# Performance work log

Hardware: AMD Instinct MI355X
Metric: run time of the kernel (lower is better)

Reference implementation:

```python
import jax, jax.numpy as jnp
import numpy as np

B, L, N, H, HU = 512, 16, 10000, 128, 128

def _rn(k, shape, s=0.05):
    return jax.random.normal(k, shape, jnp.float32) * s

def setup_inputs():
    ks = jax.random.split(jax.random.key(0), 26)
    return dict(
        x=jax.random.normal(ks[0], (B, 2), jnp.float32),
        t0_res=jax.random.normal(ks[1], (B, 1), jnp.float32),
        node_inputs=jax.random.normal(ks[2], (B, 2 * L, N), jnp.float32),
        tau_inputs=jax.random.normal(ks[3], (B, L, 1), jnp.float32),
        end=jax.random.normal(ks[4], (B, 2), jnp.float32),
        coords=jax.random.normal(ks[5], (B, 2 * L, 2), jnp.float32),
        Wx1=_rn(ks[6], (1, 2)), Wx2=_rn(ks[7], (H, 1)), bx2=_rn(ks[8], (H,)),
        Wres=_rn(ks[9], (H, 1)), bres=_rn(ks[10], (H,)),
        Wnode=_rn(ks[11], (H, N)),
        Wtau=_rn(ks[12], (H, 1)), btau=_rn(ks[13], (H,)),
        Wend1=_rn(ks[14], (1, 2)), Wend2=_rn(ks[15], (H, 1)), bend2=_rn(ks[16], (H,)),
        Wcoord=_rn(ks[17], (H, 2)),
        lstm_Wih=_rn(ks[18], (7, 4 * H, H)), lstm_Whh=_rn(ks[19], (7, 4 * H, H)),
        lstm_bih=_rn(ks[20], (7, 4 * H)), lstm_bhh=_rn(ks[21], (7, 4 * H)),
        head_W1=_rn(ks[22], (7, HU, H)), head_b1=_rn(ks[23], (7, HU)),
        head_W2=_rn(ks[24], (7, 1, HU)), head_b2=_rn(ks[25], (7, 1)),
    )

def _lstm_last(s, Wih, Whh, bih, bhh):
    # s: [T, B, H] (time-first, like torch LSTM default). PyTorch gate order: i, f, g, o.
    h0 = jnp.zeros((s.shape[1], Whh.shape[1]), s.dtype)
    def step(carry, xt):
        h, c = carry
        g = xt @ Wih.T + h @ Whh.T + (bih + bhh)
        i, f, gg, o = jnp.split(g, 4, axis=-1)
        c = jax.nn.sigmoid(f) * c + jax.nn.sigmoid(i) * jnp.tanh(gg)
        h = jax.nn.sigmoid(o) * jnp.tanh(c)
        return (h, c), None
    (h, _), _ = jax.lax.scan(step, (h0, h0), s)
    return h  # last output == last hidden state

def _forward(x, t0_res, node_inputs, tau_inputs, end, coords,
             Wx1, Wx2, bx2, Wres, bres, Wnode, Wtau, btau,
             Wend1, Wend2, bend2, Wcoord,
             lstm_Wih, lstm_Whh, lstm_bih, lstm_bhh,
             head_W1, head_b1, head_W2, head_b2):
    xh = jnp.tanh((x @ Wx1.T) @ Wx2.T + bx2)        # [B,H]
    t0h = jnp.tanh(t0_res @ Wres.T + bres)          # [B,H]
    nodeh = node_inputs @ Wnode.T                   # [B,2L,H] (dominant memory-bound GEMM)
    tauh = jnp.tanh(tau_inputs @ Wtau.T + btau)     # [B,L,H]
    endh = (end @ Wend1.T) @ Wend2.T + bend2        # [B,H]
    coordh = coords @ Wcoord.T                      # [B,2L,H]
    ne, no = nodeh[:, 0::2], nodeh[:, 1::2]         # even/odd walk nodes [B,L,H]
    ce, co = coordh[:, 0::2], coordh[:, 1::2]
    def interleave(parts):  # k x [B,L,H] -> time-first [k*L, B, H], per-step order preserved
        s = jnp.stack(parts, axis=2)
        return jnp.swapaxes(s.reshape(s.shape[0], -1, s.shape[-1]), 0, 1)
    pre = jnp.stack([xh, t0h], axis=0)  # [2,B,H]
    suf = endh[None]                    # [1,B,H]
    seqs = [
        jnp.concatenate([pre, interleave([tauh, ne, ce, no, co]), suf], 0),  # all        T=5L+3
        jnp.concatenate([pre, interleave([tauh]), suf], 0),                  # time       T=L+3
        jnp.swapaxes(nodeh, 0, 1),                                           # node       T=2L
        jnp.swapaxes(coordh, 0, 1),                                          # coord      T=2L
        jnp.concatenate([pre, interleave([tauh, ne, no]), suf], 0),          # node_time  T=3L+3
        interleave([ne, ce, no, co]),                                        # node_coord T=4L
        jnp.concatenate([pre, interleave([tauh, ce, co]), suf], 0),          # time_coord T=3L+3
    ]
    outs = []
    for k, s in enumerate(seqs):
        h = _lstm_last(s, lstm_Wih[k], lstm_Whh[k], lstm_bih[k], lstm_bhh[k])
        outs.append(jnp.tanh(h @ head_W1[k].T + head_b1[k]) @ head_W2[k].T + head_b2[k])
    return tuple(outs)  # matches torch return order: all, time, node, coord, node_time, node_coord, time_coord

def reference(x, t0_res, node_inputs, tau_inputs, end, coords,
              Wx1, Wx2, bx2, Wres, bres, Wnode, Wtau, btau,
              Wend1, Wend2, bend2, Wcoord,
              lstm_Wih, lstm_Whh, lstm_bih, lstm_bhh,
              head_W1, head_b1, head_W2, head_b2):
    return _forward(x, t0_res, node_inputs, tau_inputs, end, coords,
                    Wx1, Wx2, bx2, Wres, bres, Wnode, Wtau, btau,
                    Wend1, Wend2, bend2, Wcoord,
                    lstm_Wih, lstm_Whh, lstm_bih, lstm_bhh,
                    head_W1, head_b1, head_W2, head_b2)
```

## Files before the change

kernel.cpp:

```cpp
#include <hip/hip_runtime.h>
#include <hip/hip_fp16.h>

typedef _Float16 f16;
typedef _Float16 f16x8 __attribute__((ext_vector_type(8)));
typedef float f32x4 __attribute__((ext_vector_type(4)));

#define NB 512
#define NL 16
#define NK 10000
#define NH 128
#define NSF 316
#define NT 79

__device__ __forceinline__ float fast_exp2(float x) {
#if __has_builtin(__builtin_amdgcn_exp2f)
  return __builtin_amdgcn_exp2f(x);
#else
  return exp2f(x);
#endif
}
__device__ __forceinline__ float fast_rcp(float x) {
#if __has_builtin(__builtin_amdgcn_rcpf)
  return __builtin_amdgcn_rcpf(x);
#else
  return 1.f / x;
#endif
}
__device__ __forceinline__ float sigf(float x) {
  return fast_rcp(1.f + fast_exp2(-1.44269504f * x));
}
__device__ __forceinline__ float tanh_fast(float x) {
  return 2.f * fast_rcp(1.f + fast_exp2(-2.88539008f * x)) - 1.f;
}

__global__ void prep_kernel(
    const float* __restrict__ x, const float* __restrict__ t0,
    const float* __restrict__ tau, const float* __restrict__ endi,
    const float* __restrict__ coords,
    const float* __restrict__ Wx1, const float* __restrict__ Wx2,
    const float* __restrict__ bx2, const float* __restrict__ Wres,
    const float* __restrict__ bres, const float* __restrict__ Wnode,
    const float* __restrict__ Wtau, const float* __restrict__ btau,
    const float* __restrict__ Wend1, const float* __restrict__ Wend2,
    const float* __restrict__ bend2, const float* __restrict__ Wcoord,
    const float* __restrict__ Wih, const float* __restrict__ Whh,
    const float* __restrict__ bih, const float* __restrict__ bhh,
    f16* __restrict__ xh, f16* __restrict__ t0h, f16* __restrict__ endh,
    f16* __restrict__ tauh, f16* __restrict__ coordh, f16* __restrict__ Wf,
    f16* __restrict__ Wih16, f16* __restrict__ Whh16, float* __restrict__ bsum) {
  const int tid0 = blockIdx.x * blockDim.x + threadIdx.x;
  const int stride = gridDim.x * blockDim.x;

  const int nWf = NSF * 4096;
  const int nW = 7 * 512 * NH;
  const int nb = 7 * 512;
  const int nxh = NB * NH;
  const int ntau = NB * NL * NH;
  const int nco = NB * 2 * NL * NH;

  for (int i = tid0; i < nWf; i += stride) {
    const int s = i >> 12, r = i & 4095;
    const int nt = r >> 9, l2 = r & 511;
    const int lane = l2 >> 3, e = l2 & 7;
    const int kg = lane >> 4, lr = lane & 15;
    const int col = nt * 16 + lr;
    const int k = s * 32 + kg * 8 + e;
    Wf[i] = (k < NK) ? (f16)Wnode[(size_t)col * NK + k] : (f16)0.f;
  }
  for (int i = tid0; i < nW; i += stride) {
    Wih16[i] = (f16)Wih[i];
    Whh16[i] = (f16)Whh[i];
  }
  for (int i = tid0; i < nb; i += stride) bsum[i] = bih[i] + bhh[i];
  for (int i = tid0; i < nxh; i += stride) {
    const int b = i >> 7, h = i & 127;
    const float s = x[2 * b] * Wx1[0] + x[2 * b + 1] * Wx1[1];
    xh[i] = (f16)tanhf(s * Wx2[h] + bx2[h]);
    t0h[i] = (f16)tanhf(t0[b] * Wres[h] + bres[h]);
    const float e = endi[2 * b] * Wend1[0] + endi[2 * b + 1] * Wend1[1];
    endh[i] = (f16)(e * Wend2[h] + bend2[h]);
  }
  for (int i = tid0; i < ntau; i += stride) {
    const int h = i & 127, bl = i >> 7;
    tauh[i] = (f16)tanhf(tau[bl] * Wtau[h] + btau[h]);
  }
  for (int i = tid0; i < nco; i += stride) {
    const int h = i & 127, br = i >> 7;
    coordh[i] = (f16)(coords[2 * br] * Wcoord[2 * h] +
                      coords[2 * br + 1] * Wcoord[2 * h + 1]);
  }
}

__global__ __launch_bounds__(512, 2) void node_gemm(const float* __restrict__ A,
                                                    const f16* __restrict__ Wf,
                                                    f16* __restrict__ Cn) {
  __shared__ char lds[4][32768];
  const int tid = threadIdx.x;
  const int w = tid >> 6, l = tid & 63;
  const int lr = l & 15, kg = l >> 4;
  const int r0 = blockIdx.x * 64;
  char* lds0 = &lds[0][0];

  const char* ap[4];
  int bnd[4], wdo[4];
#pragma unroll
  for (int i = 0; i < 4; i++) {
    const int row = w * 8 + i * 2 + (l >> 5);
    const int off = (l & 31) * 16;
    ap[i] = (const char*)A + (size_t)(r0 + row) * 40000 + off;
    bnd[i] = 39984 - off;
    wdo[i] = row * 512 + (off ^ ((row & 7) << 4));
  }

  const int kw = w & 1, cp = w >> 1;
  int rdoA[4][2][2];
#pragma unroll
  for (int rg = 0; rg < 4; rg++) {
    const int row = rg * 16 + lr;
    const int sw = (row & 7) << 4;
#pragma unroll
    for (int ks = 0; ks < 2; ks++)
#pragma unroll
      for (int h = 0; h < 2; h++)
        rdoA[rg][ks][h] =
            row * 512 + ((kw * 256 + ks * 128 + kg * 32 + h * 16) ^ sw);
  }

  f32x4 acc[4][2];
#pragma unroll
  for (int rg = 0; rg < 4; rg++)
#pragma unroll
    for (int j = 0; j < 2; j++) {
      f32x4 z = {0.f, 0.f, 0.f, 0.f};
      acc[rg][j] = z;
    }

  auto loadA = [&](int t, f32x4 (&r)[4]) {
    const int tb = t * 512;
#pragma unroll
    for (int i = 0; i < 4; i++) {
      const int off = tb < bnd[i] ? tb : bnd[i];
      r[i] = *(const f32x4*)(ap[i] + off);
    }
  };

  auto dswrite = [&](int t, const f32x4 (&r)[4]) {
    char* db = lds0 + (t & 3) * 32768;
#pragma unroll
    for (int i = 0; i < 4; i++) *(f32x4*)(db + wdo[i]) = r[i];
  };

  auto loadB = [&](int t, f16x8 (&B)[2][2]) {
    const f16* bp = Wf + (size_t)(4 * t + 2 * kw) * 4096 + cp * 1024 + l * 8;
#pragma unroll
    for (int j = 0; j < 2; j++)
#pragma unroll
      for (int ks = 0; ks < 2; ks++)
        B[j][ks] = *(const f16x8*)(bp + (size_t)ks * 4096 + j * 512);
  };

  auto compute = [&](int t, const f16x8 (&B)[2][2]) {
    const char* cb = lds0 + (t & 3) * 32768;
#pragma unroll
    for (int ks = 0; ks < 2; ks++)
#pragma unroll
      for (int rg = 0; rg < 4; rg++) {
        const f32x4 a0 = *(const f32x4*)(cb + rdoA[rg][ks][0]);
        const f32x4 a1 = *(const f32x4*)(cb + rdoA[rg][ks][1]);
        f16x8 af;
        af[0] = (f16)a0[0]; af[1] = (f16)a0[1];
        af[2] = (f16)a0[2]; af[3] = (f16)a0[3];
        af[4] = (f16)a1[0]; af[5] = (f16)a1[1];
        af[6] = (f16)a1[2]; af[7] = (f16)a1[3];
#pragma unroll
        for (int j = 0; j < 2; j++)
          acc[rg][j] = __builtin_amdgcn_mfma_f32_16x16x32_f16(
              af, B[j][ks], acc[rg][j], 0, 0, 0);
      }
  };

  f32x4 RA0[4], RA1[4];
  f16x8 B0[2][2], B1[2][2];

  loadA(0, RA0);
  loadB(0, B0);
  loadA(1, RA1);

  for (int e = 0; e + 1 < NT; e += 2) {
    asm volatile("s_waitcnt vmcnt(4)" ::: "memory");
    dswrite(e, RA0);
    loadB(e + 1, B1);
    loadA(e + 2, RA0);
    asm volatile("s_waitcnt lgkmcnt(0)" ::: "memory");
    __builtin_amdgcn_s_barrier();
    compute(e, B0);
    asm volatile("s_waitcnt vmcnt(4)" ::: "memory");
    dswrite(e + 1, RA1);
    loadB(e + 2, B0);
    if (e + 3 < NT) loadA(e + 3, RA1);
    asm volatile("s_waitcnt lgkmcnt(0)" ::: "memory");
    __builtin_amdgcn_s_barrier();
    compute(e + 1, B1);
  }
  asm volatile("s_waitcnt vmcnt(0)" ::: "memory");
  dswrite(NT - 1, RA0);
  asm volatile("s_waitcnt lgkmcnt(0)" ::: "memory");
  __builtin_amdgcn_s_barrier();
  compute(NT - 1, B0);

  __syncthreads();
  if (kw == 1) {
#pragma unroll
    for (int rg = 0; rg < 4; rg++)
#pragma unroll
      for (int j = 0; j < 2; j++) {
        const int tl = cp * 8 + rg * 2 + j;
        *(f32x4*)(lds0 + tl * 1024 + l * 16) = acc[rg][j];
      }
  }
  __syncthreads();
  if (kw == 0) {
#pragma unroll
    for (int rg = 0; rg < 4; rg++)
#pragma unroll
      for (int j = 0; j < 2; j++) {
        const int tl = cp * 8 + rg * 2 + j;
        const f32x4 p = *(const f32x4*)(lds0 + tl * 1024 + l * 16);
        const f32x4 s = acc[rg][j] + p;
        f16* crow =
            Cn + (size_t)(r0 + rg * 16 + kg * 4) * NH + cp * 32 + j * 16 + lr;
#pragma unroll
        for (int jr = 0; jr < 4; jr++) crow[(size_t)jr * NH] = (f16)s[jr];
      }
  }
}

__global__ __launch_bounds__(512, 2) void lstm_run(
    const f16* __restrict__ xh, const f16* __restrict__ t0h,
    const f16* __restrict__ endh, const f16* __restrict__ tauh,
    const f16* __restrict__ nodeh, const f16* __restrict__ coordh,
    const f16* __restrict__ Wih16, const f16* __restrict__ Whh16,
    const float* __restrict__ bsum, const float* __restrict__ hW1,
    const float* __restrict__ hb1, const float* __restrict__ hW2,
    const float* __restrict__ hb2, float* __restrict__ out) {
  __shared__ f16 hbuf[2][16 * NH];
  __shared__ float hu[16 * NH];

  const int k = blockIdx.x >> 5;
  const int b0 = (blockIdx.x & 31) << 4;
  const int w = threadIdx.x >> 6;
  const int l = threadIdx.x & 63;
  const int lr = l & 15, kg = l >> 4;

  int len;
  switch (k) {
    case 0: len = 83; break;
    case 1: len = 19; break;
    case 2: len = 32; break;
    case 3: len = 32; break;
    case 4: len = 51; break;
    case 5: len = 64; break;
    default: len = 51; break;
  }

  auto xptr = [&](int t) -> const f16* {
    const f16* cb; int bstr, idx;
    if (k == 2) { cb = nodeh; bstr = 32 * NH; idx = t; }
    else if (k == 3) { cb = coordh; bstr = 32 * NH; idx = t; }
    else if (k == 5) {
      const int q = t >> 2, r = t & 3;
      cb = (r == 0 || r == 2) ? nodeh : coordh;
      bstr = 32 * NH;
      idx = 2 * q + ((r >= 2) ? 1 : 0);
    } else {
      if (t == 0) { cb = xh; bstr = NH; idx = 0; }
      else if (t == 1) { cb = t0h; bstr = NH; idx = 0; }
      else if (t == len - 1) { cb = endh; bstr = NH; idx = 0; }
      else {
        const int u = t - 2;
        if (k == 0) {
          const int q = u / 5, r = u - 5 * q;
          if (r == 0) { cb = tauh; bstr = 16 * NH; idx = q; }
          else if (r == 1) { cb = nodeh; bstr = 32 * NH; idx = 2 * q; }
          else if (r == 2) { cb = coordh; bstr = 32 * NH; idx = 2 * q; }
          else if (r == 3) { cb = nodeh; bstr = 32 * NH; idx = 2 * q + 1; }
          else { cb = coordh; bstr = 32 * NH; idx = 2 * q + 1; }
        } else if (k == 1) { cb = tauh; bstr = 16 * NH; idx = u; }
        else if (k == 4) {
          const int q = u / 3, r = u - 3 * q;
          if (r == 0) { cb = tauh; bstr = 16 * NH; idx = q; }
          else { cb = nodeh; bstr = 32 * NH; idx = 2 * q + (r - 1); }
        } else {
          const int q = u / 3, r = u - 3 * q;
          if (r == 0) { cb = tauh; bstr = 16 * NH; idx = q; }
          else { cb = coordh; bstr = 32 * NH; idx = 2 * q + (r - 1); }
        }
      }
    }
    return cb + (size_t)(b0 + lr) * bstr + idx * NH + kg * 8;
  };

  f16x8 Wh[4][4], Wi[4][4];
  float bias[4];
  {
    const f16* whb = Whh16 + (size_t)k * 512 * NH;
    const f16* wib = Wih16 + (size_t)k * 512 * NH;
#pragma unroll
    for (int g = 0; g < 4; g++) {
      const int col = g * 128 + w * 16 + lr;
      bias[g] = bsum[k * 512 + col];
#pragma unroll
      for (int kc = 0; kc < 4; kc++) {
        Wh[kc][g] = *(const f16x8*)(whb + (size_t)col * NH + kc * 32 + kg * 8);
        Wi[kc][g] = *(const f16x8*)(wib + (size_t)col * NH + kc * 32 + kg * 8);
      }
    }
  }

  char* lds0 = (char*)&hbuf[0][0];
  *(unsigned long long*)(lds0 + threadIdx.x * 8) = 0ull;
  __syncthreads();

  float c[4] = {0, 0, 0, 0};

  int rdo[4];
#pragma unroll
  for (int kc = 0; kc < 4; kc++) {
    const int colb = (kc * 32 + kg * 8) * 2;
    rdo[kc] = lr * 256 + (colb ^ ((lr & 7) << 4));
  }
  int wro[4];
#pragma unroll
  for (int jr = 0; jr < 4; jr++) {
    const int hrow = kg * 4 + jr;
    const int hcol = w * 16 + lr;
    wro[jr] = hrow * 256 + ((hcol * 2) ^ ((hrow & 7) << 4));
  }

  f16x8 axc[4];
  {
    const f16* xp = xptr(0);
#pragma unroll
    for (int kc = 0; kc < 4; kc++) axc[kc] = *(const f16x8*)(xp + kc * 32);
  }

  int cur = 0;
  for (int t = 0; t < len; t++) {
    char* rb = lds0 + cur * 4096;
    f16x8 ah[4];
#pragma unroll
    for (int kc = 0; kc < 4; kc++) ah[kc] = *(const f16x8*)(rb + rdo[kc]);

    f16x8 axn[4];
    if (t + 1 < len) {
      const f16* xp = xptr(t + 1);
#pragma unroll
      for (int kc = 0; kc < 4; kc++) axn[kc] = *(const f16x8*)(xp + kc * 32);
    }

    f32x4 acc[4];
#pragma unroll
    for (int g = 0; g < 4; g++) {
      f32x4 binit = {bias[g], bias[g], bias[g], bias[g]};
      acc[g] = binit;
    }
#pragma unroll
    for (int kc = 0; kc < 4; kc++)
#pragma unroll
      for (int g = 0; g < 4; g++)
        acc[g] = __builtin_amdgcn_mfma_f32_16x16x32_f16(axc[kc], Wi[kc][g], acc[g], 0, 0, 0);
#pragma unroll
    for (int kc = 0; kc < 4; kc++)
#pragma unroll
      for (int g = 0; g < 4; g++)
        acc[g] = __builtin_amdgcn_mfma_f32_16x16x32_f16(ah[kc], Wh[kc][g], acc[g], 0, 0, 0);

    char* wb = lds0 + (cur ^ 1) * 4096;
#pragma unroll
    for (int jr = 0; jr < 4; jr++) {
      const float iv = acc[0][jr];
      const float fv = acc[1][jr];
      const float gv = acc[2][jr];
      const float ov = acc[3][jr];
      const float cn = sigf(fv) * c[jr] + sigf(iv) * tanh_fast(gv);
      c[jr] = cn;
      const float hn = sigf(ov) * tanh_fast(cn);
      *(f16*)(wb + wro[jr]) = (f16)hn;
    }
    __syncthreads();
#pragma unroll
    for (int kc = 0; kc < 4; kc++) axc[kc] = axn[kc];
    cur ^= 1;
  }

  {
    char* rb = lds0 + cur * 4096;
    f16x8 ah[4];
#pragma unroll
    for (int kc = 0; kc < 4; kc++) ah[kc] = *(const f16x8*)(rb + rdo[kc]);
    const float* W1 = hW1 + (size_t)k * NH * NH;
    const int col = w * 16 + lr;
    f32x4 hacc;
    {
      const float b1 = hb1[k * NH + col];
      f32x4 binit = {b1, b1, b1, b1};
      hacc = binit;
    }
#pragma unroll
    for (int kc = 0; kc < 4; kc++) {
      const float* wrow = W1 + (size_t)col * NH + kc * 32 + kg * 8;
      const f32x4 w0 = *(const f32x4*)(wrow);
      const f32x4 w1 = *(const f32x4*)(wrow + 4);
      f16x8 wv;
      wv[0] = (f16)w0[0]; wv[1] = (f16)w0[1]; wv[2] = (f16)w0[2]; wv[3] = (f16)w0[3];
      wv[4] = (f16)w1[0]; wv[5] = (f16)w1[1]; wv[6] = (f16)w1[2]; wv[7] = (f16)w1[3];
      hacc = __builtin_amdgcn_mfma_f32_16x16x32_f16(ah[kc], wv, hacc, 0, 0, 0);
    }
#pragma unroll
    for (int jr = 0; jr < 4; jr++)
      hu[(kg * 4 + jr) * NH + col] = tanh_fast(hacc[jr]);
  }
  __syncthreads();
  if (w == 0) {
    const int b = l >> 2, part = l & 3;
    const float* W2 = hW2 + (size_t)k * NH;
    float s = 0.f;
#pragma unroll
    for (int j = 0; j < 32; j++)
      s += hu[b * NH + part * 32 + j] * W2[part * 32 + j];
    s += __shfl_xor(s, 1);
    s += __shfl_xor(s, 2);
    if (part == 0) out[k * NB + b0 + b] = s + hb2[k];
  }
}

extern "C" void kernel_launch(void* const* d_in, const int* in_sizes, int n_in,
                              void* d_out, int out_size, void* d_ws, size_t ws_size,
                              hipStream_t stream) {
  (void)in_sizes; (void)n_in; (void)out_size; (void)ws_size;
  const float* x = (const float*)d_in[0];
  const float* t0 = (const float*)d_in[1];
  const float* node = (const float*)d_in[2];
  const float* tau = (const float*)d_in[3];
  const float* endi = (const float*)d_in[4];
  const float* coords = (const float*)d_in[5];
  const float* Wx1 = (const float*)d_in[6];
  const float* Wx2 = (const float*)d_in[7];
  const float* bx2 = (const float*)d_in[8];
  const float* Wres = (const float*)d_in[9];
  const float* bres = (const float*)d_in[10];
  const float* Wnode = (const float*)d_in[11];
  const float* Wtau = (const float*)d_in[12];
  const float* btau = (const float*)d_in[13];
  const float* Wend1 = (const float*)d_in[14];
  const float* Wend2 = (const float*)d_in[15];
  const float* bend2 = (const float*)d_in[16];
  const float* Wcoord = (const float*)d_in[17];
  const float* Wih = (const float*)d_in[18];
  const float* Whh = (const float*)d_in[19];
  const float* bih = (const float*)d_in[20];
  const float* bhh = (const float*)d_in[21];
  const float* hW1 = (const float*)d_in[22];
  const float* hb1 = (const float*)d_in[23];
  const float* hW2 = (const float*)d_in[24];
  const float* hb2 = (const float*)d_in[25];

  char* ws = (char*)d_ws;
  f16* xh = (f16*)ws;      ws += (size_t)NB * NH * 2;
  f16* t0h = (f16*)ws;     ws += (size_t)NB * NH * 2;
  f16* endh = (f16*)ws;    ws += (size_t)NB * NH * 2;
  f16* tauh = (f16*)ws;    ws += (size_t)NB * NL * NH * 2;
  f16* nodeh = (f16*)ws;   ws += (size_t)NB * 2 * NL * NH * 2;
  f16* coordh = (f16*)ws;  ws += (size_t)NB * 2 * NL * NH * 2;
  f16* Wf = (f16*)ws;      ws += (size_t)NSF * 4096 * 2;
  f16* Wih16 = (f16*)ws;   ws += (size_t)7 * 512 * NH * 2;
  f16* Whh16 = (f16*)ws;   ws += (size_t)7 * 512 * NH * 2;
  float* bsum = (float*)ws;

  prep_kernel<<<1024, 256, 0, stream>>>(
      x, t0, tau, endi, coords, Wx1, Wx2, bx2, Wres, bres, Wnode, Wtau, btau,
      Wend1, Wend2, bend2, Wcoord, Wih, Whh, bih, bhh,
      xh, t0h, endh, tauh, coordh, Wf, Wih16, Whh16, bsum);
  node_gemm<<<256, 512, 0, stream>>>(node, Wf, nodeh);
  lstm_run<<<224, 512, 0, stream>>>(xh, t0h, endh, tauh, nodeh, coordh,
                                    Wih16, Whh16, bsum, hW1, hb1, hW2, hb2,
                                    (float*)d_out);
}
```

Before: 259.0 us.

## Deepen A-operand prefetch to two-tile bursts with nontemporal loads

```diff
diff --git a/kernel.cpp b/kernel.cpp
--- a/kernel.cpp
+++ b/kernel.cpp
@@ -9,8 +9,8 @@
 #define NL 16
 #define NK 10000
 #define NH 128
-#define NSF 316
-#define NT 79
+#define NSF 320
+#define NT 80
 
 __device__ __forceinline__ float fast_exp2(float x) {
 #if __has_builtin(__builtin_amdgcn_exp2f)
@@ -135,12 +135,14 @@
       acc[rg][j] = z;
     }
 
-  auto loadA = [&](int t, f32x4 (&r)[4]) {
-    const int tb = t * 512;
+  auto burstA = [&](int t, f32x4 (&ra)[4], f32x4 (&rb)[4]) {
+    const int tb0 = t * 512, tb1 = tb0 + 512;
 #pragma unroll
     for (int i = 0; i < 4; i++) {
-      const int off = tb < bnd[i] ? tb : bnd[i];
-      r[i] = *(const f32x4*)(ap[i] + off);
+      ra[i] = __builtin_nontemporal_load(
+          (const f32x4*)(ap[i] + (tb0 < bnd[i] ? tb0 : bnd[i])));
+      rb[i] = __builtin_nontemporal_load(
+          (const f32x4*)(ap[i] + (tb1 < bnd[i] ? tb1 : bnd[i])));
     }
   };
 
@@ -179,34 +181,38 @@
       }
   };
 
-  f32x4 RA0[4], RA1[4];
+  f32x4 RA0[4], RA1[4], RB0[4], RB1[4];
   f16x8 B0[2][2], B1[2][2];
 
-  loadA(0, RA0);
+#define PBODY(E, C0, C1, VM1S, VM2S, DOB, DOL)                        \
+  do {                                                                \
+    dswrite((E), C0);                                                 \
+    dswrite((E) + 1, C1);                                             \
+    loadB((E) + 1, B1);                                               \
+    if (DOB) burstA((E) + 4, C0, C1);                                 \
+    asm volatile("s_waitcnt lgkmcnt(0)" ::: "memory");                \
+    __builtin_amdgcn_s_barrier();                                     \
+    asm volatile("s_waitcnt vmcnt(" VM1S ")" ::: "memory");           \
+    compute((E), B0);                                                 \
+    if (DOL) loadB((E) + 2, B0);                                      \
+    asm volatile("s_waitcnt vmcnt(" VM2S ")" ::: "memory");           \
+    compute((E) + 1, B1);                                             \
+  } while (0)
+
+  burstA(0, RA0, RA1);
   loadB(0, B0);
-  loadA(1, RA1);
-
-  for (int e = 0; e + 1 < NT; e += 2) {
-    asm volatile("s_waitcnt vmcnt(4)" ::: "memory");
-    dswrite(e, RA0);
-    loadB(e + 1, B1);
-    loadA(e + 2, RA0);
-    asm volatile("s_waitcnt lgkmcnt(0)" ::: "memory");
-    __builtin_amdgcn_s_barrier();
-    compute(e, B0);
-    asm volatile("s_waitcnt vmcnt(4)" ::: "memory");
-    dswrite(e + 1, RA1);
-    loadB(e + 2, B0);
-    if (e + 3 < NT) loadA(e + 3, RA1);
-    asm volatile("s_waitcnt lgkmcnt(0)" ::: "memory");
-    __builtin_amdgcn_s_barrier();
-    compute(e + 1, B1);
-  }
-  asm volatile("s_waitcnt vmcnt(0)" ::: "memory");
-  dswrite(NT - 1, RA0);
-  asm volatile("s_waitcnt lgkmcnt(0)" ::: "memory");
-  __builtin_amdgcn_s_barrier();
-  compute(NT - 1, B0);
+  burstA(2, RB0, RB1);
+  asm volatile("s_waitcnt vmcnt(12)" ::: "memory");
+
+  PBODY(0, RA0, RA1, "20", "12", true, true);
+  PBODY(2, RB0, RB1, "12", "12", true, true);
+  for (int e = 4; e <= 72; e += 4) {
+    PBODY(e, RA0, RA1, "12", "12", true, true);
+    PBODY(e + 2, RB0, RB1, "12", "12", true, true);
+  }
+  PBODY(76, RA0, RA1, "4", "4", false, true);
+  PBODY(78, RB0, RB1, "4", "0", false, false);
+#undef PBODY
 
   __syncthreads();
   if (kw == 1) {
```

After: 245.4 us. 1.06x faster.
